# Performance work log

Hardware: AMD Instinct MI355X
Metric: run time of the kernel (lower is better)

The kernel has to match this reference:

```python
import jax, jax.numpy as jnp
import numpy as np

DT = 0.01
T, B, I, H, O = 512, 128, 256, 1024, 256


def setup_inputs() -> dict:
    key = jax.random.key(0)
    ks = jax.random.split(key, 9)
    def xavier(k, out_f, in_f):
        lim = np.sqrt(6.0 / (in_f + out_f)).astype(np.float32)
        return jax.random.uniform(k, (out_f, in_f), jnp.float32, -lim, lim)
    return {
        "x": jax.random.normal(ks[0], (T, B, I), jnp.float32),
        "W_h": xavier(ks[1], H, I + H),                      # HRCell linear, no bias
        "gain": jnp.ones((H,), jnp.float32),
        "omega": jax.random.uniform(ks[2], (H,), jnp.float32, 10.0, 50.0),
        "b_offset": jax.random.uniform(ks[3], (H,), jnp.float32, 1.0, 6.0),
        "W_o": xavier(ks[4], H, H),                          # LICell linear, no bias
        "tau_mem": 20.0 + 5.0 * jax.random.normal(ks[5], (H,), jnp.float32),
        "W_out": xavier(ks[6], O, H),                        # readout Linear
        "b_out": jnp.zeros((O,), jnp.float32),
    }


def reference(x, W_h, gain, omega, b_offset, W_o, tau_mem, W_out, b_out):
    om = jnp.abs(omega)
    om2 = om * om
    b = om2 * 0.005 + jnp.abs(b_offset)          # damping coefficient per unit
    alpha = jnp.exp(-1.0 / jnp.abs(tau_mem))     # leaky-integrator decay
    Bsz = x.shape[1]
    Hd = W_h.shape[0]
    Od = W_out.shape[0]

    def step(carry, x_t):
        hu, hv, ou, acc = carry
        # HRCell: linear on concat(input, hidden_u), then harmonic update
        in_sum = jnp.concatenate([x_t, hu], axis=1) @ W_h.T   # [B, H]
        hv = hv + hu * DT
        hu = hu + in_sum * DT - b * hu * (2.0 * DT) - om2 * hv * DT
        hu = hu * gain                                        # normalize=False path
        # LICell: leaky integrator on projected hidden
        ou = ou * alpha + (hu @ W_o.T) * (1.0 - alpha)
        # readout, summed over time
        acc = acc + ou @ W_out.T + b_out
        return (hu, hv, ou, acc), None

    z = jnp.zeros((Bsz, Hd), x.dtype)
    init = (z, z, z, jnp.zeros((Bsz, Od), x.dtype))
    (hu, hv, ou, acc), _ = jax.lax.scan(step, init, x)
    return acc
```

## Files before the change

kernel.cpp:

```cpp
#include <hip/hip_runtime.h>
#include <math.h>

#define DT 0.01f
constexpr int T = 512, B = 128, I = 256, H = 1024, O = 256;
constexpr int K = I + H;
constexpr int NKS_H = K / 32;
constexpr int NKS_O = H / 32;

constexpr size_t OFF_OSUM  = 0;
constexpr size_t OFF_HUH0  = OFF_OSUM + (size_t)B * H;
constexpr size_t OFF_HUL0  = OFF_HUH0 + (size_t)B * H / 2;
constexpr size_t OFF_HUH1  = OFF_HUL0 + (size_t)B * H / 2;
constexpr size_t OFF_HUL1  = OFF_HUH1 + (size_t)B * H / 2;
constexpr size_t OFF_COEF  = OFF_HUL1 + (size_t)B * H / 2;
constexpr size_t OFF_FLAGS = OFF_COEF + 5 * (size_t)H;
constexpr size_t OFF_WHH   = OFF_FLAGS + 4096;
constexpr size_t OFF_WHL   = OFF_WHH + 64 * 40 * 64 * 8 / 2;
constexpr size_t OFF_WOH   = OFF_WHL + 64 * 40 * 64 * 8 / 2;
constexpr size_t OFF_WOL   = OFF_WOH + 64 * 32 * 64 * 8 / 2;

constexpr int SM_WHH  = 0;
constexpr int SM_REDS = 81920;
constexpr int SM_REDP = 90368;
constexpr int SM_BYTES = 98816;

typedef __attribute__((ext_vector_type(8))) short short8v;
typedef __attribute__((ext_vector_type(4))) float f32x4;

static __device__ inline short f2bf(float f) {
    unsigned u = __builtin_bit_cast(unsigned, f);
    u += 0x7fffu + ((u >> 16) & 1u);
    return (short)(u >> 16);
}
static __device__ inline float bf2f(short s) {
    return __builtin_bit_cast(float, ((unsigned)(unsigned short)s) << 16);
}

__global__ __launch_bounds__(256)
void init_kernel(float* __restrict__ ws, const float* __restrict__ omega,
                 const float* __restrict__ b_offset, const float* __restrict__ tau_mem,
                 const float* __restrict__ gain) {
    size_t tid = (size_t)blockIdx.x * blockDim.x + threadIdx.x;
    size_t stride = (size_t)gridDim.x * blockDim.x;
    for (size_t i = tid; i < (size_t)B * H; i += stride) ws[OFF_HUH0 + i] = 0.0f;
    for (size_t i = tid; i < 4096; i += stride) ws[OFF_FLAGS + i] = 0.0f;
    if (tid < H) {
        float om  = fabsf(omega[tid]);
        float om2 = om * om;
        float bb  = om2 * 0.005f + fabsf(b_offset[tid]);
        float al  = expf(-1.0f / fabsf(tau_mem[tid]));
        float g   = gain[tid];
        ws[OFF_COEF + 0 * H + tid] = g * (1.0f - 2.0f * bb * DT);
        ws[OFF_COEF + 1 * H + tid] = g * DT;
        ws[OFF_COEF + 2 * H + tid] = g * om2 * DT;
        ws[OFF_COEF + 3 * H + tid] = al;
        ws[OFF_COEF + 4 * H + tid] = 1.0f - al;
    }
}

template <int NKS, int KD>
__global__ __launch_bounds__(256)
void convert_kernel(const float* __restrict__ W, short* __restrict__ WH,
                    short* __restrict__ WL) {
    int g = blockIdx.x * 256 + threadIdx.x;
    int lane = g & 63;
    int ks = (g >> 6) % NKS;
    int cg = g / (NKS * 64);
    int col = cg * 16 + (lane & 15);
    int k = ks * 32 + ((lane >> 4) << 3);
    const float* src = W + (size_t)col * KD + k;
    short8v hi, lo;
    #pragma unroll
    for (int j = 0; j < 8; ++j) {
        float v = src[j];
        short h = f2bf(v);
        hi[j] = h;
        lo[j] = f2bf(v - bf2f(h));
    }
    *(short8v*)(WH + (size_t)g * 8) = hi;
    *(short8v*)(WL + (size_t)g * 8) = lo;
}

__global__ __launch_bounds__(512)
void rnn_persist(const float* __restrict__ x, float* __restrict__ ws) {
    extern __shared__ char sm[];
    float* redS = (float*)(sm + SM_REDS);
    float* redP = (float*)(sm + SM_REDP);

    const float* coef = ws + OFF_COEF;
    float* osum_g = ws + OFF_OSUM;
    const short* huhS[2] = {(const short*)(ws + OFF_HUH0), (const short*)(ws + OFF_HUH1)};
    const short* hulS[2] = {(const short*)(ws + OFF_HUL0), (const short*)(ws + OFF_HUL1)};
    unsigned int* huhW[2] = {(unsigned int*)(ws + OFF_HUH0), (unsigned int*)(ws + OFF_HUH1)};
    unsigned int* hulW[2] = {(unsigned int*)(ws + OFF_HUL0), (unsigned int*)(ws + OFF_HUL1)};
    int* flags = (int*)(ws + OFF_FLAGS);

    const int wg = blockIdx.x;
    const int xcd = wg & 7, idx = wg >> 3;
    const int g = xcd * 4 + (idx & 3);
    const int rowt = idx >> 2;
    const int col0 = g * 32;
    const int row0 = rowt * 16;

    const int tid = threadIdx.x;
    const int wid = tid >> 6, lane = tid & 63;
    const int ntile = wid & 1, ksl = wid >> 1;
    const int colgrp = 2 * g + ntile;
    const int rowg = row0 + (lane & 15);
    const int koff = (lane >> 4) << 3;

    {
        const float4* srcH = (const float4*)(ws + OFF_WHH);
        float4* dH = (float4*)(sm + SM_WHH);
        for (int i = tid; i < 2 * 2560; i += 512) {
            int n = i / 2560, j = i - n * 2560;
            dH[n * 2560 + j] = srcH[(size_t)(2 * g + n) * 2560 + j];
        }
    }
    __syncthreads();

    const short8v* lWHH = (const short8v*)(sm + SM_WHH) + (size_t)ntile * 2560 + lane;
    const short8v* WHLg = (const short8v*)(ws + OFF_WHL) + (size_t)colgrp * NKS_H * 64 + lane;
    const short8v* WOHg = (const short8v*)(ws + OFF_WOH) + (size_t)colgrp * NKS_O * 64 + lane;
    const short8v* WOLg = (const short8v*)(ws + OFF_WOL) + (size_t)colgrp * NKS_O * 64 + lane;

    const int er = tid >> 4;
    const int ec0 = (tid & 15) * 2;
    const int gcol0 = col0 + ec0;
    const size_t erow = (size_t)(row0 + (er & 15));
    float k1a = 0, k1b = 0, k2a = 0, k2b = 0, k3a = 0, k3b = 0;
    float ala = 0, alb = 0, alma = 0, almb = 0;
    if (tid < 256) {
        k1a = coef[gcol0];         k1b = coef[gcol0 + 1];
        k2a = coef[H + gcol0];     k2b = coef[H + gcol0 + 1];
        k3a = coef[2 * H + gcol0]; k3b = coef[2 * H + gcol0 + 1];
        ala = coef[3 * H + gcol0]; alb = coef[3 * H + gcol0 + 1];
        alma = coef[4 * H + gcol0]; almb = coef[4 * H + gcol0 + 1];
    }
    float hva = 0, hvb = 0, oua = 0, oub = 0, osa = 0, osb = 0, hua = 0, hub = 0;

    int* myflag = flags + ((rowt * 32 + g) << 4);

    for (int s = 0; s <= T; ++s) {
        const bool last = (s == T);
        f32x4 accS = {0, 0, 0, 0}, accP = {0, 0, 0, 0};
        short8v whl[10], woh[8], wol[8];

        #pragma unroll
        for (int j = 0; j < 8; ++j) {
            woh[j] = WOHg[(ksl * 8 + j) * 64];
            wol[j] = WOLg[(ksl * 8 + j) * 64];
        }
        if (!last) {
            #pragma unroll
            for (int j = 0; j < 2; ++j) whl[j] = WHLg[(ksl * 2 + j) * 64];
            #pragma unroll
            for (int j = 0; j < 8; ++j) whl[2 + j] = WHLg[(8 + ksl * 8 + j) * 64];
            const float* xrow = x + (size_t)s * B * I + (size_t)rowg * I + koff;
            #pragma unroll
            for (int j = 0; j < 2; ++j) {
                int ks = ksl * 2 + j;
                float4 a0 = *(const float4*)(xrow + ks * 32);
                float4 a1 = *(const float4*)(xrow + ks * 32 + 4);
                float av[8] = {a0.x, a0.y, a0.z, a0.w, a1.x, a1.y, a1.z, a1.w};
                short8v ah, alv;
                #pragma unroll
                for (int q = 0; q < 8; ++q) {
                    short h = f2bf(av[q]);
                    ah[q] = h;
                    alv[q] = f2bf(av[q] - bf2f(h));
                }
                short8v ch = lWHH[ks * 64];
                short8v cl = whl[j];
                accS = __builtin_amdgcn_mfma_f32_16x16x32_bf16(ah, ch, accS, 0, 0, 0);
                accS = __builtin_amdgcn_mfma_f32_16x16x32_bf16(alv, ch, accS, 0, 0, 0);
                accS = __builtin_amdgcn_mfma_f32_16x16x32_bf16(ah, cl, accS, 0, 0, 0);
            }
        }

        if (tid < 32) {
            int* pollp = flags + ((rowt * 32 + tid) << 4);
            while (__hip_atomic_load(pollp, __ATOMIC_RELAXED, __HIP_MEMORY_SCOPE_AGENT) < s)
                __builtin_amdgcn_s_sleep(1);
        }
        __syncthreads();
        asm volatile("" ::: "memory");

        const short* hbase = huhS[s & 1] + (size_t)rowg * H + koff;
        const short* lbase = hulS[s & 1] + (size_t)rowg * H + koff;
        short8v hbuf[8], lbuf[8];
        #pragma unroll
        for (int j = 0; j < 8; ++j) {
            const short* hp = hbase + (ksl * 8 + j) * 32;
            const short* lp = lbase + (ksl * 8 + j) * 32;
            asm volatile("global_load_dwordx4 %0, %1, off sc0 sc1"
                         : "=v"(hbuf[j]) : "v"(hp));
            asm volatile("global_load_dwordx4 %0, %1, off sc0 sc1"
                         : "=v"(lbuf[j]) : "v"(lp));
        }
        if (s > 0 && tid < 256) {
            int base = er * 33 + ec0;
            float p0 = (redP[base] + redP[528 + base]) + (redP[1056 + base] + redP[1584 + base]);
            float p1 = (redP[base + 1] + redP[528 + base + 1]) + (redP[1056 + base + 1] + redP[1584 + base + 1]);
            float o0 = oua * ala + p0 * alma; oua = o0; osa += o0;
            float o1 = oub * alb + p1 * almb; oub = o1; osb += o1;
        }

        if (!last) {
            asm volatile("s_waitcnt vmcnt(8)");
            __builtin_amdgcn_sched_barrier(0);
            #pragma unroll
            for (int j = 0; j < 4; ++j) {
                short8v ch = lWHH[(8 + ksl * 8 + j) * 64];
                short8v cl = whl[2 + j];
                accS = __builtin_amdgcn_mfma_f32_16x16x32_bf16(hbuf[j], ch, accS, 0, 0, 0);
                accS = __builtin_amdgcn_mfma_f32_16x16x32_bf16(lbuf[j], ch, accS, 0, 0, 0);
                accS = __builtin_amdgcn_mfma_f32_16x16x32_bf16(hbuf[j], cl, accS, 0, 0, 0);
            }
            asm volatile("s_waitcnt vmcnt(0)");
            __builtin_amdgcn_sched_barrier(0);
            #pragma unroll
            for (int j = 4; j < 8; ++j) {
                short8v ch = lWHH[(8 + ksl * 8 + j) * 64];
                short8v cl = whl[2 + j];
                accS = __builtin_amdgcn_mfma_f32_16x16x32_bf16(hbuf[j], ch, accS, 0, 0, 0);
                accS = __builtin_amdgcn_mfma_f32_16x16x32_bf16(lbuf[j], ch, accS, 0, 0, 0);
                accS = __builtin_amdgcn_mfma_f32_16x16x32_bf16(hbuf[j], cl, accS, 0, 0, 0);
            }
            #pragma unroll
            for (int r = 0; r < 4; ++r) {
                int crow = ((lane >> 4) << 2) + r;
                redS[ksl * 528 + crow * 33 + ntile * 16 + (lane & 15)] = accS[r];
            }
            __syncthreads();

            if (tid < 256) {
                int base = er * 33 + ec0;
                float s0 = (redS[base] + redS[528 + base]) + (redS[1056 + base] + redS[1584 + base]);
                float s1 = (redS[base + 1] + redS[528 + base + 1]) + (redS[1056 + base + 1] + redS[1584 + base + 1]);
                float hvn0 = hva + hua * DT;
                float hun0 = k1a * hua + k2a * s0 - k3a * hvn0;
                hva = hvn0; hua = hun0;
                float hvn1 = hvb + hub * DT;
                float hun1 = k1b * hub + k2b * s1 - k3b * hvn1;
                hvb = hvn1; hub = hun1;
                short h0 = f2bf(hun0), h1 = f2bf(hun1);
                short l0 = f2bf(hun0 - bf2f(h0)), l1 = f2bf(hun1 - bf2f(h1));
                unsigned hpack = (unsigned)(unsigned short)h0 | ((unsigned)(unsigned short)h1 << 16);
                unsigned lpack = (unsigned)(unsigned short)l0 | ((unsigned)(unsigned short)l1 << 16);
                size_t off32 = (erow * H + gcol0) >> 1;
                __hip_atomic_store(huhW[(s + 1) & 1] + off32, hpack, __ATOMIC_RELAXED, __HIP_MEMORY_SCOPE_AGENT);
                __hip_atomic_store(hulW[(s + 1) & 1] + off32, lpack, __ATOMIC_RELAXED, __HIP_MEMORY_SCOPE_AGENT);
            }
            asm volatile("s_waitcnt vmcnt(0)" ::: "memory");
            __syncthreads();
            if (tid == 0)
                __hip_atomic_store(myflag, s + 1, __ATOMIC_RELAXED, __HIP_MEMORY_SCOPE_AGENT);
        } else {
            asm volatile("s_waitcnt vmcnt(0)");
            __builtin_amdgcn_sched_barrier(0);
            __syncthreads();
        }

        #pragma unroll
        for (int j = 0; j < 8; ++j) {
            accP = __builtin_amdgcn_mfma_f32_16x16x32_bf16(hbuf[j], woh[j], accP, 0, 0, 0);
            accP = __builtin_amdgcn_mfma_f32_16x16x32_bf16(lbuf[j], woh[j], accP, 0, 0, 0);
            accP = __builtin_amdgcn_mfma_f32_16x16x32_bf16(hbuf[j], wol[j], accP, 0, 0, 0);
        }
        #pragma unroll
        for (int r = 0; r < 4; ++r) {
            int crow = ((lane >> 4) << 2) + r;
            redP[ksl * 528 + crow * 33 + ntile * 16 + (lane & 15)] = accP[r];
        }
    }

    __syncthreads();
    if (tid < 256) {
        int base = er * 33 + ec0;
        float p0 = (redP[base] + redP[528 + base]) + (redP[1056 + base] + redP[1584 + base]);
        float p1 = (redP[base + 1] + redP[528 + base + 1]) + (redP[1056 + base + 1] + redP[1584 + base + 1]);
        float o0 = oua * ala + p0 * alma; osa += o0;
        float o1 = oub * alb + p1 * almb; osb += o1;
        osum_g[erow * H + gcol0] = osa;
        osum_g[erow * H + gcol0 + 1] = osb;
    }
}

__global__ __launch_bounds__(256)
void readout_kernel(const float* __restrict__ ou_sum, const float* __restrict__ W_out,
                    const float* __restrict__ b_out, float* __restrict__ out) {
    constexpr int KC = 128, BT = 32, CT = 16;
    __shared__ float act[BT][KC + 4];
    __shared__ float w[CT][KC + 4];
    int wg = blockIdx.x;
    int bt = wg & 3, cg = wg >> 2;
    int row0 = bt * BT, col0 = cg * CT;
    int tid = threadIdx.x;
    int c = tid & 15, rr = tid >> 4;

    float4 acc0 = {0, 0, 0, 0}, acc1 = {0, 0, 0, 0};
    for (int kc = 0; kc < H / KC; ++kc) {
        int k0 = kc * KC;
        for (int i = tid; i < BT * (KC / 4); i += 256) {
            int r = i >> 5, c4 = (i & 31) * 4;
            *(float4*)&act[r][c4] = *(const float4*)&ou_sum[(size_t)(row0 + r) * H + k0 + c4];
        }
        for (int i = tid; i < CT * (KC / 4); i += 256) {
            int r = i >> 5, c4 = (i & 31) * 4;
            *(float4*)&w[r][c4] = *(const float4*)&W_out[(size_t)(col0 + r) * H + k0 + c4];
        }
        __syncthreads();
        #pragma unroll
        for (int k4 = 0; k4 < KC / 4; ++k4) {
            float4 a0 = *(const float4*)&act[rr][k4 * 4];
            float4 a1 = *(const float4*)&act[rr + 16][k4 * 4];
            float4 w0 = *(const float4*)&w[c][k4 * 4];
            acc0.x = fmaf(a0.x, w0.x, acc0.x); acc0.y = fmaf(a0.y, w0.y, acc0.y);
            acc0.z = fmaf(a0.z, w0.z, acc0.z); acc0.w = fmaf(a0.w, w0.w, acc0.w);
            acc1.x = fmaf(a1.x, w0.x, acc1.x); acc1.y = fmaf(a1.y, w0.y, acc1.y);
            acc1.z = fmaf(a1.z, w0.z, acc1.z); acc1.w = fmaf(a1.w, w0.w, acc1.w);
        }
        __syncthreads();
    }
    float v0 = (acc0.x + acc0.y) + (acc0.z + acc0.w);
    float v1 = (acc1.x + acc1.y) + (acc1.z + acc1.w);
    int gcol = col0 + c;
    float bo = b_out[gcol] * (float)T;
    out[(size_t)(row0 + rr) * O + gcol] = v0 + bo;
    out[(size_t)(row0 + rr + 16) * O + gcol] = v1 + bo;
}

extern "C" void kernel_launch(void* const* d_in, const int* in_sizes, int n_in,
                              void* d_out, int out_size, void* d_ws, size_t ws_size,
                              hipStream_t stream) {
    const float* x        = (const float*)d_in[0];
    const float* W_h      = (const float*)d_in[1];
    const float* gain     = (const float*)d_in[2];
    const float* omega    = (const float*)d_in[3];
    const float* b_offset = (const float*)d_in[4];
    const float* W_o      = (const float*)d_in[5];
    const float* tau_mem  = (const float*)d_in[6];
    const float* W_out    = (const float*)d_in[7];
    const float* b_out    = (const float*)d_in[8];
    float* ws  = (float*)d_ws;
    float* out = (float*)d_out;

    init_kernel<<<512, 256, 0, stream>>>(ws, omega, b_offset, tau_mem, gain);
    convert_kernel<40, K><<<640, 256, 0, stream>>>(
        W_h, (short*)(ws + OFF_WHH), (short*)(ws + OFF_WHL));
    convert_kernel<32, H><<<512, 256, 0, stream>>>(
        W_o, (short*)(ws + OFF_WOH), (short*)(ws + OFF_WOL));

    rnn_persist<<<256, 512, SM_BYTES, stream>>>(x, ws);

    readout_kernel<<<64, 256, 0, stream>>>(ws + OFF_OSUM, W_out, b_out, out);
}
```

Before: 3.855 ms.

## Split persistent RNN into 512 smaller workgroups with fused hidden/projection MFMA loop

Doubles the persistent grid to 512 workgroups of 256 threads, each handling 8 batch rows across both column tiles, with launch bounds set for two workgroups per CU. The hidden-weight and output-projection MFMAs now share a single pass over the loaded hu fragments, the hidden-weight low parts are held in registers, the x-part weights are streamed from global memory, and redP is double-buffered so the leaky-integrator update moves to the next step. The aim is more parallelism per step and overlap of the W_o projection with the hidden recurrence. In exchange it wastes half of each 16-row MFMA tile on 8 rows, doubles the number of flags to poll, and re-reads W_o from global memory every step.

```diff
diff --git a/kernel.cpp b/kernel.cpp
--- a/kernel.cpp
+++ b/kernel.cpp
@@ -4,8 +4,6 @@
 #define DT 0.01f
 constexpr int T = 512, B = 128, I = 256, H = 1024, O = 256;
 constexpr int K = I + H;
-constexpr int NKS_H = K / 32;
-constexpr int NKS_O = H / 32;
 
 constexpr size_t OFF_OSUM  = 0;
 constexpr size_t OFF_HUH0  = OFF_OSUM + (size_t)B * H;
@@ -14,15 +12,15 @@
 constexpr size_t OFF_HUL1  = OFF_HUH1 + (size_t)B * H / 2;
 constexpr size_t OFF_COEF  = OFF_HUL1 + (size_t)B * H / 2;
 constexpr size_t OFF_FLAGS = OFF_COEF + 5 * (size_t)H;
-constexpr size_t OFF_WHH   = OFF_FLAGS + 4096;
+constexpr size_t OFF_WHH   = OFF_FLAGS + 8192;
 constexpr size_t OFF_WHL   = OFF_WHH + 64 * 40 * 64 * 8 / 2;
 constexpr size_t OFF_WOH   = OFF_WHL + 64 * 40 * 64 * 8 / 2;
 constexpr size_t OFF_WOL   = OFF_WOH + 64 * 32 * 64 * 8 / 2;
 
 constexpr int SM_WHH  = 0;
-constexpr int SM_REDS = 81920;
-constexpr int SM_REDP = 90368;
-constexpr int SM_BYTES = 98816;
+constexpr int SM_REDS = 65536;
+constexpr int SM_REDP = 69760;
+constexpr int SM_BYTES = 78208;
 
 typedef __attribute__((ext_vector_type(8))) short short8v;
 typedef __attribute__((ext_vector_type(4))) float f32x4;
@@ -43,7 +41,7 @@
     size_t tid = (size_t)blockIdx.x * blockDim.x + threadIdx.x;
     size_t stride = (size_t)gridDim.x * blockDim.x;
     for (size_t i = tid; i < (size_t)B * H; i += stride) ws[OFF_HUH0 + i] = 0.0f;
-    for (size_t i = tid; i < 4096; i += stride) ws[OFF_FLAGS + i] = 0.0f;
+    for (size_t i = tid; i < 8192; i += stride) ws[OFF_FLAGS + i] = 0.0f;
     if (tid < H) {
         float om  = fabsf(omega[tid]);
         float om2 = om * om;
@@ -81,7 +79,7 @@
     *(short8v*)(WL + (size_t)g * 8) = lo;
 }
 
-__global__ __launch_bounds__(512)
+__global__ __launch_bounds__(256, 2)
 void rnn_persist(const float* __restrict__ x, float* __restrict__ ws) {
     extern __shared__ char sm[];
     float* redS = (float*)(sm + SM_REDS);
@@ -99,82 +97,85 @@
     const int xcd = wg & 7, idx = wg >> 3;
     const int g = xcd * 4 + (idx & 3);
     const int rowt = idx >> 2;
-    const int col0 = g * 32;
-    const int row0 = rowt * 16;
+    const int col0 = g * 32, row0 = rowt * 8;
 
     const int tid = threadIdx.x;
-    const int wid = tid >> 6, lane = tid & 63;
-    const int ntile = wid & 1, ksl = wid >> 1;
-    const int colgrp = 2 * g + ntile;
-    const int rowg = row0 + (lane & 15);
+    const int ksl = tid >> 6;
+    const int lane = tid & 63;
+    const int rowg = row0 + (lane & 7);
     const int koff = (lane >> 4) << 3;
 
     {
-        const float4* srcH = (const float4*)(ws + OFF_WHH);
-        float4* dH = (float4*)(sm + SM_WHH);
-        for (int i = tid; i < 2 * 2560; i += 512) {
-            int n = i / 2560, j = i - n * 2560;
-            dH[n * 2560 + j] = srcH[(size_t)(2 * g + n) * 2560 + j];
+        const float4* src = (const float4*)(ws + OFF_WHH);
+        float4* dst = (float4*)sm;
+        for (int i = tid; i < 4096; i += 256) {
+            int n = i >> 11, rem = i & 2047;
+            dst[i] = src[((size_t)(2 * g + n) * 40 + 8) * 64 + rem];
+        }
+    }
+    short8v whl[16];
+    {
+        const short8v* pL = (const short8v*)(ws + OFF_WHL) + lane;
+        #pragma unroll
+        for (int jj = 0; jj < 8; ++jj) {
+            whl[jj * 2 + 0] = pL[((size_t)(2 * g + 0) * 40 + 8 + ksl * 8 + jj) * 64];
+            whl[jj * 2 + 1] = pL[((size_t)(2 * g + 1) * 40 + 8 + ksl * 8 + jj) * 64];
         }
     }
     __syncthreads();
 
-    const short8v* lWHH = (const short8v*)(sm + SM_WHH) + (size_t)ntile * 2560 + lane;
-    const short8v* WHLg = (const short8v*)(ws + OFF_WHL) + (size_t)colgrp * NKS_H * 64 + lane;
-    const short8v* WOHg = (const short8v*)(ws + OFF_WOH) + (size_t)colgrp * NKS_O * 64 + lane;
-    const short8v* WOLg = (const short8v*)(ws + OFF_WOL) + (size_t)colgrp * NKS_O * 64 + lane;
-
-    const int er = tid >> 4;
-    const int ec0 = (tid & 15) * 2;
-    const int gcol0 = col0 + ec0;
-    const size_t erow = (size_t)(row0 + (er & 15));
-    float k1a = 0, k1b = 0, k2a = 0, k2b = 0, k3a = 0, k3b = 0;
-    float ala = 0, alb = 0, alma = 0, almb = 0;
-    if (tid < 256) {
+    const short8v* lWHH = (const short8v*)sm + lane;
+    const short8v* pOH = (const short8v*)(ws + OFF_WOH) + lane;
+    const short8v* pOL = (const short8v*)(ws + OFF_WOL) + lane;
+    const short8v* pXH = (const short8v*)(ws + OFF_WHH) + lane;
+    const short8v* pXL = (const short8v*)(ws + OFF_WHL) + lane;
+
+    const int er = (tid >> 4) & 7, cp = tid & 15;
+    const int gcol0 = col0 + cp * 2;
+    const size_t erow = (size_t)(row0 + er);
+    float k1a=0,k1b=0,k2a=0,k2b=0,k3a=0,k3b=0, ala=0,alb=0,alma=0,almb=0;
+    if (tid < 128) {
         k1a = coef[gcol0];         k1b = coef[gcol0 + 1];
         k2a = coef[H + gcol0];     k2b = coef[H + gcol0 + 1];
         k3a = coef[2 * H + gcol0]; k3b = coef[2 * H + gcol0 + 1];
         ala = coef[3 * H + gcol0]; alb = coef[3 * H + gcol0 + 1];
         alma = coef[4 * H + gcol0]; almb = coef[4 * H + gcol0 + 1];
     }
-    float hva = 0, hvb = 0, oua = 0, oub = 0, osa = 0, osb = 0, hua = 0, hub = 0;
-
+    float hva=0,hvb=0,oua=0,oub=0,osa=0,osb=0,hua=0,hub=0;
+
+    const size_t rowOffH = (size_t)rowg * H + koff;
     int* myflag = flags + ((rowt * 32 + g) << 4);
 
     for (int s = 0; s <= T; ++s) {
-        const bool last = (s == T);
-        f32x4 accS = {0, 0, 0, 0}, accP = {0, 0, 0, 0};
-        short8v whl[10], woh[8], wol[8];
-
-        #pragma unroll
-        for (int j = 0; j < 8; ++j) {
-            woh[j] = WOHg[(ksl * 8 + j) * 64];
-            wol[j] = WOLg[(ksl * 8 + j) * 64];
-        }
-        if (!last) {
-            #pragma unroll
-            for (int j = 0; j < 2; ++j) whl[j] = WHLg[(ksl * 2 + j) * 64];
-            #pragma unroll
-            for (int j = 0; j < 8; ++j) whl[2 + j] = WHLg[(8 + ksl * 8 + j) * 64];
+        const bool lastI = (s == T);
+        f32x4 accS0 = {0,0,0,0}, accS1 = {0,0,0,0};
+        f32x4 accP0 = {0,0,0,0}, accP1 = {0,0,0,0};
+
+        if (!lastI) {
             const float* xrow = x + (size_t)s * B * I + (size_t)rowg * I + koff;
             #pragma unroll
-            for (int j = 0; j < 2; ++j) {
-                int ks = ksl * 2 + j;
-                float4 a0 = *(const float4*)(xrow + ks * 32);
-                float4 a1 = *(const float4*)(xrow + ks * 32 + 4);
-                float av[8] = {a0.x, a0.y, a0.z, a0.w, a1.x, a1.y, a1.z, a1.w};
-                short8v ah, alv;
+            for (int jj = 0; jj < 2; ++jj) {
+                int xj = ksl * 2 + jj;
+                short8v wxh0 = pXH[((size_t)(2 * g + 0) * 40 + xj) * 64];
+                short8v wxh1 = pXH[((size_t)(2 * g + 1) * 40 + xj) * 64];
+                short8v wxl0 = pXL[((size_t)(2 * g + 0) * 40 + xj) * 64];
+                short8v wxl1 = pXL[((size_t)(2 * g + 1) * 40 + xj) * 64];
+                float4 a0 = *(const float4*)(xrow + xj * 32);
+                float4 a1 = *(const float4*)(xrow + xj * 32 + 4);
+                float av[8] = {a0.x,a0.y,a0.z,a0.w,a1.x,a1.y,a1.z,a1.w};
+                short8v ah, al;
                 #pragma unroll
                 for (int q = 0; q < 8; ++q) {
                     short h = f2bf(av[q]);
                     ah[q] = h;
-                    alv[q] = f2bf(av[q] - bf2f(h));
+                    al[q] = f2bf(av[q] - bf2f(h));
                 }
-                short8v ch = lWHH[ks * 64];
-                short8v cl = whl[j];
-                accS = __builtin_amdgcn_mfma_f32_16x16x32_bf16(ah, ch, accS, 0, 0, 0);
-                accS = __builtin_amdgcn_mfma_f32_16x16x32_bf16(alv, ch, accS, 0, 0, 0);
-                accS = __builtin_amdgcn_mfma_f32_16x16x32_bf16(ah, cl, accS, 0, 0, 0);
+                accS0 = __builtin_amdgcn_mfma_f32_16x16x32_bf16(ah, wxh0, accS0, 0,0,0);
+                accS0 = __builtin_amdgcn_mfma_f32_16x16x32_bf16(al, wxh0, accS0, 0,0,0);
+                accS0 = __builtin_amdgcn_mfma_f32_16x16x32_bf16(ah, wxl0, accS0, 0,0,0);
+                accS1 = __builtin_amdgcn_mfma_f32_16x16x32_bf16(ah, wxh1, accS1, 0,0,0);
+                accS1 = __builtin_amdgcn_mfma_f32_16x16x32_bf16(al, wxh1, accS1, 0,0,0);
+                accS1 = __builtin_amdgcn_mfma_f32_16x16x32_bf16(ah, wxl1, accS1, 0,0,0);
             }
         }
 
@@ -186,58 +187,82 @@
         __syncthreads();
         asm volatile("" ::: "memory");
 
-        const short* hbase = huhS[s & 1] + (size_t)rowg * H + koff;
-        const short* lbase = hulS[s & 1] + (size_t)rowg * H + koff;
-        short8v hbuf[8], lbuf[8];
+        if (s > 0 && tid < 128) {
+            const float* rp = redP + ((s - 1) & 1) * 1056 + er * 33 + cp * 2;
+            float p0 = (rp[0] + rp[264]) + (rp[528] + rp[792]);
+            float p1 = (rp[1] + rp[265]) + (rp[529] + rp[793]);
+            oua = oua * ala + p0 * alma; osa += oua;
+            oub = oub * alb + p1 * almb; osb += oub;
+        }
+
+        const short* hb_ = huhS[s & 1] + rowOffH;
+        const short* lb_ = hulS[s & 1] + rowOffH;
         #pragma unroll
-        for (int j = 0; j < 8; ++j) {
-            const short* hp = hbase + (ksl * 8 + j) * 32;
-            const short* lp = lbase + (ksl * 8 + j) * 32;
-            asm volatile("global_load_dwordx4 %0, %1, off sc0 sc1"
-                         : "=v"(hbuf[j]) : "v"(hp));
-            asm volatile("global_load_dwordx4 %0, %1, off sc0 sc1"
-                         : "=v"(lbuf[j]) : "v"(lp));
-        }
-        if (s > 0 && tid < 256) {
-            int base = er * 33 + ec0;
-            float p0 = (redP[base] + redP[528 + base]) + (redP[1056 + base] + redP[1584 + base]);
-            float p1 = (redP[base + 1] + redP[528 + base + 1]) + (redP[1056 + base + 1] + redP[1584 + base + 1]);
-            float o0 = oua * ala + p0 * alma; oua = o0; osa += o0;
-            float o1 = oub * alb + p1 * almb; oub = o1; osb += o1;
-        }
-
-        if (!last) {
-            asm volatile("s_waitcnt vmcnt(8)");
-            __builtin_amdgcn_sched_barrier(0);
-            #pragma unroll
-            for (int j = 0; j < 4; ++j) {
-                short8v ch = lWHH[(8 + ksl * 8 + j) * 64];
-                short8v cl = whl[2 + j];
-                accS = __builtin_amdgcn_mfma_f32_16x16x32_bf16(hbuf[j], ch, accS, 0, 0, 0);
-                accS = __builtin_amdgcn_mfma_f32_16x16x32_bf16(lbuf[j], ch, accS, 0, 0, 0);
-                accS = __builtin_amdgcn_mfma_f32_16x16x32_bf16(hbuf[j], cl, accS, 0, 0, 0);
-            }
-            asm volatile("s_waitcnt vmcnt(0)");
-            __builtin_amdgcn_sched_barrier(0);
-            #pragma unroll
-            for (int j = 4; j < 8; ++j) {
-                short8v ch = lWHH[(8 + ksl * 8 + j) * 64];
-                short8v cl = whl[2 + j];
-                accS = __builtin_amdgcn_mfma_f32_16x16x32_bf16(hbuf[j], ch, accS, 0, 0, 0);
-                accS = __builtin_amdgcn_mfma_f32_16x16x32_bf16(lbuf[j], ch, accS, 0, 0, 0);
-                accS = __builtin_amdgcn_mfma_f32_16x16x32_bf16(hbuf[j], cl, accS, 0, 0, 0);
-            }
+        for (int b = 0; b < 2; ++b) {
+            const int jbase = ksl * 8 + b * 4;
+            short8v woh[8], wol[8], hbuf[4], lbuf[4];
+            #pragma unroll
+            for (int jj = 0; jj < 4; ++jj) {
+                asm volatile("global_load_dwordx4 %0, %1, off" : "=v"(woh[jj*2+0]) : "v"(pOH + ((size_t)(2*g+0)*32 + jbase + jj) * 64));
+                asm volatile("global_load_dwordx4 %0, %1, off" : "=v"(woh[jj*2+1]) : "v"(pOH + ((size_t)(2*g+1)*32 + jbase + jj) * 64));
+                asm volatile("global_load_dwordx4 %0, %1, off" : "=v"(wol[jj*2+0]) : "v"(pOL + ((size_t)(2*g+0)*32 + jbase + jj) * 64));
+                asm volatile("global_load_dwordx4 %0, %1, off" : "=v"(wol[jj*2+1]) : "v"(pOL + ((size_t)(2*g+1)*32 + jbase + jj) * 64));
+            }
+            #pragma unroll
+            for (int jj = 0; jj < 4; ++jj) {
+                asm volatile("global_load_dwordx4 %0, %1, off sc0 sc1" : "=v"(hbuf[jj]) : "v"(hb_ + (jbase + jj) * 32));
+                asm volatile("global_load_dwordx4 %0, %1, off sc0 sc1" : "=v"(lbuf[jj]) : "v"(lb_ + (jbase + jj) * 32));
+            }
+            #pragma unroll
+            for (int jj = 0; jj < 4; ++jj) {
+                if (jj == 0)      { asm volatile("s_waitcnt vmcnt(6)"); }
+                else if (jj == 1) { asm volatile("s_waitcnt vmcnt(4)"); }
+                else if (jj == 2) { asm volatile("s_waitcnt vmcnt(2)"); }
+                else              { asm volatile("s_waitcnt vmcnt(0)"); }
+                __builtin_amdgcn_sched_barrier(0);
+                short8v ch0 = lWHH[((size_t)(0 * 32) + jbase + jj) * 64];
+                short8v ch1 = lWHH[((size_t)(1 * 32) + jbase + jj) * 64];
+                if (!lastI) {
+                    accS0 = __builtin_amdgcn_mfma_f32_16x16x32_bf16(hbuf[jj], ch0, accS0, 0,0,0);
+                    accS0 = __builtin_amdgcn_mfma_f32_16x16x32_bf16(lbuf[jj], ch0, accS0, 0,0,0);
+                    accS0 = __builtin_amdgcn_mfma_f32_16x16x32_bf16(hbuf[jj], whl[(b*4+jj)*2+0], accS0, 0,0,0);
+                    accS1 = __builtin_amdgcn_mfma_f32_16x16x32_bf16(hbuf[jj], ch1, accS1, 0,0,0);
+                    accS1 = __builtin_amdgcn_mfma_f32_16x16x32_bf16(lbuf[jj], ch1, accS1, 0,0,0);
+                    accS1 = __builtin_amdgcn_mfma_f32_16x16x32_bf16(hbuf[jj], whl[(b*4+jj)*2+1], accS1, 0,0,0);
+                }
+                accP0 = __builtin_amdgcn_mfma_f32_16x16x32_bf16(hbuf[jj], woh[jj*2+0], accP0, 0,0,0);
+                accP0 = __builtin_amdgcn_mfma_f32_16x16x32_bf16(lbuf[jj], woh[jj*2+0], accP0, 0,0,0);
+                accP0 = __builtin_amdgcn_mfma_f32_16x16x32_bf16(hbuf[jj], wol[jj*2+0], accP0, 0,0,0);
+                accP1 = __builtin_amdgcn_mfma_f32_16x16x32_bf16(hbuf[jj], woh[jj*2+1], accP1, 0,0,0);
+                accP1 = __builtin_amdgcn_mfma_f32_16x16x32_bf16(lbuf[jj], woh[jj*2+1], accP1, 0,0,0);
+                accP1 = __builtin_amdgcn_mfma_f32_16x16x32_bf16(hbuf[jj], wol[jj*2+1], accP1, 0,0,0);
+            }
+        }
+
+        {
+            const int crow = (lane >> 4) << 2;
+            const int cc = lane & 15;
+            float* rp = redP + (s & 1) * 1056 + ksl * 264;
             #pragma unroll
             for (int r = 0; r < 4; ++r) {
-                int crow = ((lane >> 4) << 2) + r;
-                redS[ksl * 528 + crow * 33 + ntile * 16 + (lane & 15)] = accS[r];
-            }
-            __syncthreads();
-
-            if (tid < 256) {
-                int base = er * 33 + ec0;
-                float s0 = (redS[base] + redS[528 + base]) + (redS[1056 + base] + redS[1584 + base]);
-                float s1 = (redS[base + 1] + redS[528 + base + 1]) + (redS[1056 + base + 1] + redS[1584 + base + 1]);
+                int cr = crow + r;
+                if (cr < 8) {
+                    rp[cr * 33 + cc] = accP0[r];
+                    rp[cr * 33 + 16 + cc] = accP1[r];
+                    if (!lastI) {
+                        redS[ksl * 264 + cr * 33 + cc] = accS0[r];
+                        redS[ksl * 264 + cr * 33 + 16 + cc] = accS1[r];
+                    }
+                }
+            }
+        }
+        __syncthreads();
+
+        if (!lastI) {
+            if (tid < 128) {
+                const float* rs = redS + er * 33 + cp * 2;
+                float s0 = (rs[0] + rs[264]) + (rs[528] + rs[792]);
+                float s1 = (rs[1] + rs[265]) + (rs[529] + rs[793]);
                 float hvn0 = hva + hua * DT;
                 float hun0 = k1a * hua + k2a * s0 - k3a * hvn0;
                 hva = hvn0; hua = hun0;
@@ -246,40 +271,24 @@
                 hvb = hvn1; hub = hun1;
                 short h0 = f2bf(hun0), h1 = f2bf(hun1);
                 short l0 = f2bf(hun0 - bf2f(h0)), l1 = f2bf(hun1 - bf2f(h1));
-                unsigned hpack = (unsigned)(unsigned short)h0 | ((unsigned)(unsigned short)h1 << 16);
-                unsigned lpack = (unsigned)(unsigned short)l0 | ((unsigned)(unsigned short)l1 << 16);
+                unsigned hp = (unsigned)(unsigned short)h0 | ((unsigned)(unsigned short)h1 << 16);
+                unsigned lp = (unsigned)(unsigned short)l0 | ((unsigned)(unsigned short)l1 << 16);
                 size_t off32 = (erow * H + gcol0) >> 1;
-                __hip_atomic_store(huhW[(s + 1) & 1] + off32, hpack, __ATOMIC_RELAXED, __HIP_MEMORY_SCOPE_AGENT);
-                __hip_atomic_store(hulW[(s + 1) & 1] + off32, lpack, __ATOMIC_RELAXED, __HIP_MEMORY_SCOPE_AGENT);
+                __hip_atomic_store(huhW[(s + 1) & 1] + off32, hp, __ATOMIC_RELAXED, __HIP_MEMORY_SCOPE_AGENT);
+                __hip_atomic_store(hulW[(s + 1) & 1] + off32, lp, __ATOMIC_RELAXED, __HIP_MEMORY_SCOPE_AGENT);
             }
             asm volatile("s_waitcnt vmcnt(0)" ::: "memory");
             __syncthreads();
             if (tid == 0)
                 __hip_atomic_store(myflag, s + 1, __ATOMIC_RELAXED, __HIP_MEMORY_SCOPE_AGENT);
-        } else {
-            asm volatile("s_waitcnt vmcnt(0)");
-            __builtin_amdgcn_sched_barrier(0);
-            __syncthreads();
-        }
-
-        #pragma unroll
-        for (int j = 0; j < 8; ++j) {
-            accP = __builtin_amdgcn_mfma_f32_16x16x32_bf16(hbuf[j], woh[j], accP, 0, 0, 0);
-            accP = __builtin_amdgcn_mfma_f32_16x16x32_bf16(lbuf[j], woh[j], accP, 0, 0, 0);
-            accP = __builtin_amdgcn_mfma_f32_16x16x32_bf16(hbuf[j], wol[j], accP, 0, 0, 0);
-        }
-        #pragma unroll
-        for (int r = 0; r < 4; ++r) {
-            int crow = ((lane >> 4) << 2) + r;
-            redP[ksl * 528 + crow * 33 + ntile * 16 + (lane & 15)] = accP[r];
         }
     }
 
     __syncthreads();
-    if (tid < 256) {
-        int base = er * 33 + ec0;
-        float p0 = (redP[base] + redP[528 + base]) + (redP[1056 + base] + redP[1584 + base]);
-        float p1 = (redP[base + 1] + redP[528 + base + 1]) + (redP[1056 + base + 1] + redP[1584 + base + 1]);
+    if (tid < 128) {
+        const float* rp = redP + (T & 1) * 1056 + er * 33 + cp * 2;
+        float p0 = (rp[0] + rp[264]) + (rp[528] + rp[792]);
+        float p1 = (rp[1] + rp[265]) + (rp[529] + rp[793]);
         float o0 = oua * ala + p0 * alma; osa += o0;
         float o1 = oub * alb + p1 * almb; osb += o1;
         osum_g[erow * H + gcol0] = osa;
@@ -352,7 +361,7 @@
     convert_kernel<32, H><<<512, 256, 0, stream>>>(
         W_o, (short*)(ws + OFF_WOH), (short*)(ws + OFF_WOL));
 
-    rnn_persist<<<256, 512, SM_BYTES, stream>>>(x, ws);
+    rnn_persist<<<512, 256, SM_BYTES, stream>>>(x, ws);
 
     readout_kernel<<<64, 256, 0, stream>>>(ws + OFF_OSUM, W_out, b_out, out);
 }
```

Result: slower. 7.733 ms (+100.6%).

## Assign workgroup roles by XCC id and keep recurrent weights resident on-chip

Applied to the files above, without the earlier changes.

Each workgroup reads its hardware XCC id and takes a slot from a per-XCC atomic counter, so all workgroups sharing a row tile sit on the same XCD. The hidden-state exchange can then use sc0-only loads and stores (no sc1) and stay in the shared L2 instead of going to system scope. The recurrent W_h hi/lo slices move into LDS, and the W_x and W_o fragments are loaded once into registers instead of every step, which removes per-step global weight traffic. The W_o low-part correction MFMA is dropped, giving a small precision loss in the ou projection. LDS use grows to about 148KB, and the role assignment relies on exactly 32 workgroups landing on each XCC.

```diff
diff --git a/kernel.cpp b/kernel.cpp
--- a/kernel.cpp
+++ b/kernel.cpp
@@ -4,8 +4,6 @@
 #define DT 0.01f
 constexpr int T = 512, B = 128, I = 256, H = 1024, O = 256;
 constexpr int K = I + H;
-constexpr int NKS_H = K / 32;
-constexpr int NKS_O = H / 32;
 
 constexpr size_t OFF_OSUM  = 0;
 constexpr size_t OFF_HUH0  = OFF_OSUM + (size_t)B * H;
@@ -14,15 +12,16 @@
 constexpr size_t OFF_HUL1  = OFF_HUH1 + (size_t)B * H / 2;
 constexpr size_t OFF_COEF  = OFF_HUL1 + (size_t)B * H / 2;
 constexpr size_t OFF_FLAGS = OFF_COEF + 5 * (size_t)H;
-constexpr size_t OFF_WHH   = OFF_FLAGS + 4096;
+constexpr size_t OFF_WHH   = OFF_FLAGS + 8192;
 constexpr size_t OFF_WHL   = OFF_WHH + 64 * 40 * 64 * 8 / 2;
 constexpr size_t OFF_WOH   = OFF_WHL + 64 * 40 * 64 * 8 / 2;
 constexpr size_t OFF_WOL   = OFF_WOH + 64 * 32 * 64 * 8 / 2;
 
 constexpr int SM_WHH  = 0;
-constexpr int SM_REDS = 81920;
-constexpr int SM_REDP = 90368;
-constexpr int SM_BYTES = 98816;
+constexpr int SM_WHL  = 65536;
+constexpr int SM_REDS = 131072;
+constexpr int SM_REDP = 139520;
+constexpr int SM_BYTES = 147968;
 
 typedef __attribute__((ext_vector_type(8))) short short8v;
 typedef __attribute__((ext_vector_type(4))) float f32x4;
@@ -43,7 +42,7 @@
     size_t tid = (size_t)blockIdx.x * blockDim.x + threadIdx.x;
     size_t stride = (size_t)gridDim.x * blockDim.x;
     for (size_t i = tid; i < (size_t)B * H; i += stride) ws[OFF_HUH0 + i] = 0.0f;
-    for (size_t i = tid; i < 4096; i += stride) ws[OFF_FLAGS + i] = 0.0f;
+    for (size_t i = tid; i < 8192; i += stride) ws[OFF_FLAGS + i] = 0.0f;
     if (tid < H) {
         float om  = fabsf(omega[tid]);
         float om2 = om * om;
@@ -86,6 +85,7 @@
     extern __shared__ char sm[];
     float* redS = (float*)(sm + SM_REDS);
     float* redP = (float*)(sm + SM_REDP);
+    __shared__ int role_sm;
 
     const float* coef = ws + OFF_COEF;
     float* osum_g = ws + OFF_OSUM;
@@ -94,15 +94,22 @@
     unsigned int* huhW[2] = {(unsigned int*)(ws + OFF_HUH0), (unsigned int*)(ws + OFF_HUH1)};
     unsigned int* hulW[2] = {(unsigned int*)(ws + OFF_HUL0), (unsigned int*)(ws + OFF_HUL1)};
     int* flags = (int*)(ws + OFF_FLAGS);
-
-    const int wg = blockIdx.x;
-    const int xcd = wg & 7, idx = wg >> 3;
-    const int g = xcd * 4 + (idx & 3);
-    const int rowt = idx >> 2;
-    const int col0 = g * 32;
-    const int row0 = rowt * 16;
+    int* ctr   = flags + 4096;
 
     const int tid = threadIdx.x;
+
+    if (tid == 0) {
+        unsigned xcc_;
+        asm volatile("s_getreg_b32 %0, hwreg(HW_REG_XCC_ID)" : "=s"(xcc_));
+        int slot = atomicAdd(ctr + (xcc_ & 7), 1);
+        role_sm = (int)((xcc_ & 7) * 32 + (slot & 31));
+    }
+    __syncthreads();
+    const int role = role_sm;
+    const int xcc = role >> 5;
+    const int g   = role & 31;
+    const int col0 = g * 32, row0 = xcc * 16;
+
     const int wid = tid >> 6, lane = tid & 63;
     const int ntile = wid & 1, ksl = wid >> 1;
     const int colgrp = 2 * g + ntile;
@@ -111,25 +118,35 @@
 
     {
         const float4* srcH = (const float4*)(ws + OFF_WHH);
+        const float4* srcL = (const float4*)(ws + OFF_WHL);
         float4* dH = (float4*)(sm + SM_WHH);
-        for (int i = tid; i < 2 * 2560; i += 512) {
-            int n = i / 2560, j = i - n * 2560;
-            dH[n * 2560 + j] = srcH[(size_t)(2 * g + n) * 2560 + j];
-        }
+        float4* dL = (float4*)(sm + SM_WHL);
+        for (int i = tid; i < 2 * 2048; i += 512) {
+            int n = i >> 11, rem = i & 2047;
+            dH[i] = srcH[((size_t)(2 * g + n) * 40 + 8) * 64 + rem];
+            dL[i] = srcL[((size_t)(2 * g + n) * 40 + 8) * 64 + rem];
+        }
+    }
+    short8v woh[8], wxh[2], wxl[2];
+    {
+        const short8v* WOHg = (const short8v*)(ws + OFF_WOH) + (size_t)colgrp * 32 * 64 + lane;
+        const short8v* WXH  = (const short8v*)(ws + OFF_WHH) + (size_t)colgrp * 40 * 64 + lane;
+        const short8v* WXL  = (const short8v*)(ws + OFF_WHL) + (size_t)colgrp * 40 * 64 + lane;
+        #pragma unroll
+        for (int j = 0; j < 8; ++j) woh[j] = WOHg[(ksl * 8 + j) * 64];
+        #pragma unroll
+        for (int j = 0; j < 2; ++j) { wxh[j] = WXH[(ksl * 2 + j) * 64]; wxl[j] = WXL[(ksl * 2 + j) * 64]; }
     }
     __syncthreads();
 
-    const short8v* lWHH = (const short8v*)(sm + SM_WHH) + (size_t)ntile * 2560 + lane;
-    const short8v* WHLg = (const short8v*)(ws + OFF_WHL) + (size_t)colgrp * NKS_H * 64 + lane;
-    const short8v* WOHg = (const short8v*)(ws + OFF_WOH) + (size_t)colgrp * NKS_O * 64 + lane;
-    const short8v* WOLg = (const short8v*)(ws + OFF_WOL) + (size_t)colgrp * NKS_O * 64 + lane;
+    const short8v* lWHH = (const short8v*)(sm + SM_WHH) + (size_t)ntile * 2048 + lane;
+    const short8v* lWHL = (const short8v*)(sm + SM_WHL) + (size_t)ntile * 2048 + lane;
 
     const int er = tid >> 4;
     const int ec0 = (tid & 15) * 2;
     const int gcol0 = col0 + ec0;
     const size_t erow = (size_t)(row0 + (er & 15));
-    float k1a = 0, k1b = 0, k2a = 0, k2b = 0, k3a = 0, k3b = 0;
-    float ala = 0, alb = 0, alma = 0, almb = 0;
+    float k1a=0,k1b=0,k2a=0,k2b=0,k3a=0,k3b=0, ala=0,alb=0,alma=0,almb=0;
     if (tid < 256) {
         k1a = coef[gcol0];         k1b = coef[gcol0 + 1];
         k2a = coef[H + gcol0];     k2b = coef[H + gcol0 + 1];
@@ -137,32 +154,22 @@
         ala = coef[3 * H + gcol0]; alb = coef[3 * H + gcol0 + 1];
         alma = coef[4 * H + gcol0]; almb = coef[4 * H + gcol0 + 1];
     }
-    float hva = 0, hvb = 0, oua = 0, oub = 0, osa = 0, osb = 0, hua = 0, hub = 0;
-
-    int* myflag = flags + ((rowt * 32 + g) << 4);
+    float hva=0,hvb=0,oua=0,oub=0,osa=0,osb=0,hua=0,hub=0;
+
+    int* myflag = flags + ((xcc * 32 + g) << 4);
+    const size_t rowOffH = (size_t)rowg * H + koff;
 
     for (int s = 0; s <= T; ++s) {
         const bool last = (s == T);
         f32x4 accS = {0, 0, 0, 0}, accP = {0, 0, 0, 0};
-        short8v whl[10], woh[8], wol[8];
-
-        #pragma unroll
-        for (int j = 0; j < 8; ++j) {
-            woh[j] = WOHg[(ksl * 8 + j) * 64];
-            wol[j] = WOLg[(ksl * 8 + j) * 64];
-        }
+
         if (!last) {
-            #pragma unroll
-            for (int j = 0; j < 2; ++j) whl[j] = WHLg[(ksl * 2 + j) * 64];
-            #pragma unroll
-            for (int j = 0; j < 8; ++j) whl[2 + j] = WHLg[(8 + ksl * 8 + j) * 64];
             const float* xrow = x + (size_t)s * B * I + (size_t)rowg * I + koff;
             #pragma unroll
             for (int j = 0; j < 2; ++j) {
-                int ks = ksl * 2 + j;
-                float4 a0 = *(const float4*)(xrow + ks * 32);
-                float4 a1 = *(const float4*)(xrow + ks * 32 + 4);
-                float av[8] = {a0.x, a0.y, a0.z, a0.w, a1.x, a1.y, a1.z, a1.w};
+                float4 a0 = *(const float4*)(xrow + (ksl * 2 + j) * 32);
+                float4 a1 = *(const float4*)(xrow + (ksl * 2 + j) * 32 + 4);
+                float av[8] = {a0.x,a0.y,a0.z,a0.w,a1.x,a1.y,a1.z,a1.w};
                 short8v ah, alv;
                 #pragma unroll
                 for (int q = 0; q < 8; ++q) {
@@ -170,40 +177,34 @@
                     ah[q] = h;
                     alv[q] = f2bf(av[q] - bf2f(h));
                 }
-                short8v ch = lWHH[ks * 64];
-                short8v cl = whl[j];
-                accS = __builtin_amdgcn_mfma_f32_16x16x32_bf16(ah, ch, accS, 0, 0, 0);
-                accS = __builtin_amdgcn_mfma_f32_16x16x32_bf16(alv, ch, accS, 0, 0, 0);
-                accS = __builtin_amdgcn_mfma_f32_16x16x32_bf16(ah, cl, accS, 0, 0, 0);
+                accS = __builtin_amdgcn_mfma_f32_16x16x32_bf16(ah, wxh[j], accS, 0,0,0);
+                accS = __builtin_amdgcn_mfma_f32_16x16x32_bf16(alv, wxh[j], accS, 0,0,0);
+                accS = __builtin_amdgcn_mfma_f32_16x16x32_bf16(ah, wxl[j], accS, 0,0,0);
             }
         }
 
         if (tid < 32) {
-            int* pollp = flags + ((rowt * 32 + tid) << 4);
+            int* pollp = flags + ((xcc * 32 + tid) << 4);
             while (__hip_atomic_load(pollp, __ATOMIC_RELAXED, __HIP_MEMORY_SCOPE_AGENT) < s)
                 __builtin_amdgcn_s_sleep(1);
         }
         __syncthreads();
         asm volatile("" ::: "memory");
 
-        const short* hbase = huhS[s & 1] + (size_t)rowg * H + koff;
-        const short* lbase = hulS[s & 1] + (size_t)rowg * H + koff;
+        const short* hb_ = huhS[s & 1] + rowOffH;
+        const short* lb_ = hulS[s & 1] + rowOffH;
         short8v hbuf[8], lbuf[8];
         #pragma unroll
         for (int j = 0; j < 8; ++j) {
-            const short* hp = hbase + (ksl * 8 + j) * 32;
-            const short* lp = lbase + (ksl * 8 + j) * 32;
-            asm volatile("global_load_dwordx4 %0, %1, off sc0 sc1"
-                         : "=v"(hbuf[j]) : "v"(hp));
-            asm volatile("global_load_dwordx4 %0, %1, off sc0 sc1"
-                         : "=v"(lbuf[j]) : "v"(lp));
+            asm volatile("global_load_dwordx4 %0, %1, off sc0" : "=v"(hbuf[j]) : "v"(hb_ + (ksl * 8 + j) * 32));
+            asm volatile("global_load_dwordx4 %0, %1, off sc0" : "=v"(lbuf[j]) : "v"(lb_ + (ksl * 8 + j) * 32));
         }
         if (s > 0 && tid < 256) {
-            int base = er * 33 + ec0;
-            float p0 = (redP[base] + redP[528 + base]) + (redP[1056 + base] + redP[1584 + base]);
-            float p1 = (redP[base + 1] + redP[528 + base + 1]) + (redP[1056 + base + 1] + redP[1584 + base + 1]);
-            float o0 = oua * ala + p0 * alma; oua = o0; osa += o0;
-            float o1 = oub * alb + p1 * almb; oub = o1; osb += o1;
+            const float* rp = redP + er * 33 + ec0;
+            float p0 = (rp[0] + rp[528]) + (rp[1056] + rp[1584]);
+            float p1 = (rp[1] + rp[529]) + (rp[1057] + rp[1585]);
+            oua = oua * ala + p0 * alma; osa += oua;
+            oub = oub * alb + p1 * almb; osb += oub;
         }
 
         if (!last) {
@@ -211,21 +212,21 @@
             __builtin_amdgcn_sched_barrier(0);
             #pragma unroll
             for (int j = 0; j < 4; ++j) {
-                short8v ch = lWHH[(8 + ksl * 8 + j) * 64];
-                short8v cl = whl[2 + j];
-                accS = __builtin_amdgcn_mfma_f32_16x16x32_bf16(hbuf[j], ch, accS, 0, 0, 0);
-                accS = __builtin_amdgcn_mfma_f32_16x16x32_bf16(lbuf[j], ch, accS, 0, 0, 0);
-                accS = __builtin_amdgcn_mfma_f32_16x16x32_bf16(hbuf[j], cl, accS, 0, 0, 0);
+                short8v ch = lWHH[(ksl * 8 + j) * 64];
+                short8v cl = lWHL[(ksl * 8 + j) * 64];
+                accS = __builtin_amdgcn_mfma_f32_16x16x32_bf16(hbuf[j], ch, accS, 0,0,0);
+                accS = __builtin_amdgcn_mfma_f32_16x16x32_bf16(lbuf[j], ch, accS, 0,0,0);
+                accS = __builtin_amdgcn_mfma_f32_16x16x32_bf16(hbuf[j], cl, accS, 0,0,0);
             }
             asm volatile("s_waitcnt vmcnt(0)");
             __builtin_amdgcn_sched_barrier(0);
             #pragma unroll
             for (int j = 4; j < 8; ++j) {
-                short8v ch = lWHH[(8 + ksl * 8 + j) * 64];
-                short8v cl = whl[2 + j];
-                accS = __builtin_amdgcn_mfma_f32_16x16x32_bf16(hbuf[j], ch, accS, 0, 0, 0);
-                accS = __builtin_amdgcn_mfma_f32_16x16x32_bf16(lbuf[j], ch, accS, 0, 0, 0);
-                accS = __builtin_amdgcn_mfma_f32_16x16x32_bf16(hbuf[j], cl, accS, 0, 0, 0);
+                short8v ch = lWHH[(ksl * 8 + j) * 64];
+                short8v cl = lWHL[(ksl * 8 + j) * 64];
+                accS = __builtin_amdgcn_mfma_f32_16x16x32_bf16(hbuf[j], ch, accS, 0,0,0);
+                accS = __builtin_amdgcn_mfma_f32_16x16x32_bf16(lbuf[j], ch, accS, 0,0,0);
+                accS = __builtin_amdgcn_mfma_f32_16x16x32_bf16(hbuf[j], cl, accS, 0,0,0);
             }
             #pragma unroll
             for (int r = 0; r < 4; ++r) {
@@ -235,9 +236,9 @@
             __syncthreads();
 
             if (tid < 256) {
-                int base = er * 33 + ec0;
-                float s0 = (redS[base] + redS[528 + base]) + (redS[1056 + base] + redS[1584 + base]);
-                float s1 = (redS[base + 1] + redS[528 + base + 1]) + (redS[1056 + base + 1] + redS[1584 + base + 1]);
+                const float* rs = redS + er * 33 + ec0;
+                float s0 = (rs[0] + rs[528]) + (rs[1056] + rs[1584]);
+                float s1 = (rs[1] + rs[529]) + (rs[1057] + rs[1585]);
                 float hvn0 = hva + hua * DT;
                 float hun0 = k1a * hua + k2a * s0 - k3a * hvn0;
                 hva = hvn0; hua = hun0;
@@ -246,11 +247,13 @@
                 hvb = hvn1; hub = hun1;
                 short h0 = f2bf(hun0), h1 = f2bf(hun1);
                 short l0 = f2bf(hun0 - bf2f(h0)), l1 = f2bf(hun1 - bf2f(h1));
-                unsigned hpack = (unsigned)(unsigned short)h0 | ((unsigned)(unsigned short)h1 << 16);
-                unsigned lpack = (unsigned)(unsigned short)l0 | ((unsigned)(unsigned short)l1 << 16);
+                unsigned hp = (unsigned)(unsigned short)h0 | ((unsigned)(unsigned short)h1 << 16);
+                unsigned lp = (unsigned)(unsigned short)l0 | ((unsigned)(unsigned short)l1 << 16);
                 size_t off32 = (erow * H + gcol0) >> 1;
-                __hip_atomic_store(huhW[(s + 1) & 1] + off32, hpack, __ATOMIC_RELAXED, __HIP_MEMORY_SCOPE_AGENT);
-                __hip_atomic_store(hulW[(s + 1) & 1] + off32, lpack, __ATOMIC_RELAXED, __HIP_MEMORY_SCOPE_AGENT);
+                unsigned int* hp_ = huhW[(s + 1) & 1] + off32;
+                unsigned int* lp_ = hulW[(s + 1) & 1] + off32;
+                asm volatile("global_store_dword %0, %1, off sc0" :: "v"(hp_), "v"(hp) : "memory");
+                asm volatile("global_store_dword %0, %1, off sc0" :: "v"(lp_), "v"(lp) : "memory");
             }
             asm volatile("s_waitcnt vmcnt(0)" ::: "memory");
             __syncthreads();
@@ -264,9 +267,8 @@
 
         #pragma unroll
         for (int j = 0; j < 8; ++j) {
-            accP = __builtin_amdgcn_mfma_f32_16x16x32_bf16(hbuf[j], woh[j], accP, 0, 0, 0);
-            accP = __builtin_amdgcn_mfma_f32_16x16x32_bf16(lbuf[j], woh[j], accP, 0, 0, 0);
-            accP = __builtin_amdgcn_mfma_f32_16x16x32_bf16(hbuf[j], wol[j], accP, 0, 0, 0);
+            accP = __builtin_amdgcn_mfma_f32_16x16x32_bf16(hbuf[j], woh[j], accP, 0,0,0);
+            accP = __builtin_amdgcn_mfma_f32_16x16x32_bf16(lbuf[j], woh[j], accP, 0,0,0);
         }
         #pragma unroll
         for (int r = 0; r < 4; ++r) {
@@ -277,9 +279,9 @@
 
     __syncthreads();
     if (tid < 256) {
-        int base = er * 33 + ec0;
-        float p0 = (redP[base] + redP[528 + base]) + (redP[1056 + base] + redP[1584 + base]);
-        float p1 = (redP[base + 1] + redP[528 + base + 1]) + (redP[1056 + base + 1] + redP[1584 + base + 1]);
+        const float* rp = redP + er * 33 + ec0;
+        float p0 = (rp[0] + rp[528]) + (rp[1056] + rp[1584]);
+        float p1 = (rp[1] + rp[529]) + (rp[1057] + rp[1585]);
         float o0 = oua * ala + p0 * alma; osa += o0;
         float o1 = oub * alb + p1 * almb; osb += o1;
         osum_g[erow * H + gcol0] = osa;
```

New measurement: 3.717 ms. 3.6% less time.
